# Kernel optimization log

Hardware: AMD Instinct MI355X
Metric: run time of the kernel (lower is better)

## Reference

```python
import jax, jax.numpy as jnp
import numpy as np

B, T, N, F_OUT, K, HID = 8, 12, 4096, 12, 3, 64
HALF = T // 2


def setup_inputs() -> dict:
    key = jax.random.key(0)
    ks = jax.random.split(key, 7)
    return {
        "x": jax.random.normal(ks[0], (B, T, N, 1), jnp.float32),
        "adj": jax.random.normal(ks[1], (K, N, N), jnp.float32) / np.float32(np.sqrt(N)),
        "cheb_w": jax.random.normal(ks[2], (HID, K), jnp.float32) / np.float32(np.sqrt(K)),
        "gcn_w": jax.random.normal(ks[3], (F_OUT, T, 1, HID), jnp.float32) / np.float32(np.sqrt(T * HID)),
        "gcn_b": jnp.zeros((F_OUT,), jnp.float32),
        "glu1_w": jax.random.normal(ks[4], (F_OUT, HALF, 3, 3), jnp.float32) / np.float32(np.sqrt(HALF * 9)),
        "glu1_b": jnp.zeros((F_OUT,), jnp.float32),
        "glu2_w": jax.random.normal(ks[5], (F_OUT, HALF, 3, 3), jnp.float32) / np.float32(np.sqrt(HALF * 9)),
        "glu2_b": jnp.zeros((F_OUT,), jnp.float32),
    }


def _dilated_conv(x, w, b):
    # Conv2d(kernel=3, dilation=2, padding=2) on (B, C, N, 1)
    y = jax.lax.conv_general_dilated(
        x, w, window_strides=(1, 1), padding=((2, 2), (2, 2)),
        rhs_dilation=(2, 2), dimension_numbers=("NCHW", "OIHW", "NCHW"))
    return y + b[None, :, None, None]


def reference(x, adj, cheb_w, gcn_w, gcn_b, glu1_w, glu1_b, glu2_w, glu2_b):
    # --- ChebConv (vectorized over the per-channel Python loop) ---
    # x: (B, T, N, 1), adj: (K, N, N) -> y: (B, T, N, K)
    y = jnp.einsum("knm,btm->btnk", adj, x[..., 0])
    # Linear(K -> HID, no bias) + ReLU -> cheb: (B, T, N, HID)
    cheb = jax.nn.relu(jnp.einsum("btnk,ok->btno", y, cheb_w))
    # --- gcn_conv: Conv2d(T -> F_OUT, kernel (1, HID)) -> (B, F_OUT, N, 1) ---
    sgc = jnp.einsum("btnj,otj->bon", cheb, gcn_w[:, :, 0, :]) + gcn_b[None, :, None]
    sgc = sgc[..., None]
    # --- GLU path: split history in half, dilated convs, a * sigmoid(g) ---
    x_u, x_v = x[:, :HALF], x[:, HALF:]
    a = _dilated_conv(x_u, glu1_w, glu1_b)
    g = _dilated_conv(x_v, glu2_w, glu2_b)
    x_glu = a * jax.nn.sigmoid(g)
    return x_glu + sgc
```

## Files before the change

### kernel.cpp

```cpp
#include <hip/hip_runtime.h>
#include <hip/hip_bf16.h>
#include <math.h>

#define NNODES 4096
#define NCOLS  96
#define NROWS  12288

typedef __attribute__((ext_vector_type(8))) short short8;
typedef __attribute__((ext_vector_type(4))) float float4v;

__global__ void probe_dtype(const unsigned int* __restrict__ aw, int* __restrict__ flag) {
    int tid = threadIdx.x;
    unsigned w = aw[tid];
    unsigned e = (w >> 7) & 0xffu;
    bool insane = (e >= 0xC0u) || (e <= 0x30u);
    unsigned long long m = __ballot(insane);
    if (tid == 0) flag[0] = (__popcll(m) >= 16) ? 1 : 0;
}

__device__ __forceinline__ float ldf(const void* p, size_t i, int isf32) {
    return isf32 ? ((const float*)p)[i]
                 : __bfloat162float(((const __hip_bfloat16*)p)[i]);
}

__device__ __forceinline__ void ld8(float* d, const void* p, size_t e, int isf32) {
    if (isf32) {
        const float4* s = (const float4*)((const float*)p + e);
        float4 f0 = s[0], f1 = s[1];
        d[0] = f0.x; d[1] = f0.y; d[2] = f0.z; d[3] = f0.w;
        d[4] = f1.x; d[5] = f1.y; d[6] = f1.z; d[7] = f1.w;
    } else {
        const __hip_bfloat16* s = (const __hip_bfloat16*)p + e;
#pragma unroll
        for (int j = 0; j < 8; j++) d[j] = __bfloat162float(s[j]);
    }
}

__device__ __forceinline__ void st4bf(__hip_bfloat16* d, float4 f) {
    __align__(8) __hip_bfloat16 t[4];
    t[0] = __float2bfloat16(f.x); t[1] = __float2bfloat16(f.y);
    t[2] = __float2bfloat16(f.z); t[3] = __float2bfloat16(f.w);
    *(uint2*)d = *(const uint2*)t;
}

__global__ __launch_bounds__(256) void gemm_y(
    const void* __restrict__ adjv, const void* __restrict__ xv,
    float* __restrict__ yws, const int* __restrict__ flag)
{
    __shared__ __align__(16) __hip_bfloat16 As[64][72];
    __shared__ __align__(16) __hip_bfloat16 Xs[96][72];

    const int tid = threadIdx.x;
    const int isf32 = flag[0];
    const size_t row0 = (size_t)blockIdx.x * 64;

    const int wv = tid >> 6;
    const int ln = tid & 63;
    const int fr = ln & 15;
    const int fq = ln >> 4;

    float4v acc[6];
#pragma unroll
    for (int i = 0; i < 6; i++) acc[i] = (float4v){0.f, 0.f, 0.f, 0.f};

    if (isf32) {
        const float* adjf = (const float*)adjv;
        const float* xf   = (const float*)xv;
        const int ar = tid >> 2;
        const int ac = (tid & 3) * 16;

        float4 ra[4], rx[6];
#pragma unroll
        for (int i = 0; i < 4; i++)
            ra[i] = *(const float4*)(adjf + (row0 + ar) * NNODES + ac + i * 4);
#pragma unroll
        for (int s = 0; s < 6; s++) {
            int idx = tid + s * 256;
            int r = idx >> 4, c = (idx & 15) * 4;
            rx[s] = *(const float4*)(xf + (size_t)r * NNODES + c);
        }

        for (int kk = 0; kk < NNODES; kk += 64) {
            __syncthreads();
#pragma unroll
            for (int i = 0; i < 4; i++) st4bf(&As[ar][ac + i * 4], ra[i]);
#pragma unroll
            for (int s = 0; s < 6; s++) {
                int idx = tid + s * 256;
                int r = idx >> 4, c = (idx & 15) * 4;
                st4bf(&Xs[r][c], rx[s]);
            }
            if (kk + 64 < NNODES) {
                int kn = kk + 64;
#pragma unroll
                for (int i = 0; i < 4; i++)
                    ra[i] = *(const float4*)(adjf + (row0 + ar) * NNODES + kn + ac + i * 4);
#pragma unroll
                for (int s = 0; s < 6; s++) {
                    int idx = tid + s * 256;
                    int r = idx >> 4, c = (idx & 15) * 4;
                    rx[s] = *(const float4*)(xf + (size_t)r * NNODES + kn + c);
                }
            }
            __syncthreads();
#pragma unroll
            for (int kq = 0; kq < 2; kq++) {
                short8 a = *(const short8*)(&As[wv * 16 + fr][kq * 32 + fq * 8]);
#pragma unroll
                for (int ct = 0; ct < 6; ct++) {
                    short8 b = *(const short8*)(&Xs[ct * 16 + fr][kq * 32 + fq * 8]);
                    acc[ct] = __builtin_amdgcn_mfma_f32_16x16x32_bf16(a, b, acc[ct], 0, 0, 0);
                }
            }
        }
    } else {
        const __hip_bfloat16* adjb = (const __hip_bfloat16*)adjv;
        const __hip_bfloat16* xb   = (const __hip_bfloat16*)xv;
        const int ar = tid >> 2;
        const int ac = (tid & 3) * 16;
        for (int kk = 0; kk < NNODES; kk += 64) {
            __syncthreads();
            *(uint4*)(&As[ar][ac]) =
                *(const uint4*)(adjb + (row0 + ar) * NNODES + kk + ac);
            *(uint4*)(&As[ar][ac + 8]) =
                *(const uint4*)(adjb + (row0 + ar) * NNODES + kk + ac + 8);
#pragma unroll
            for (int s = 0; s < 3; s++) {
                int idx = tid + s * 256;
                int r = idx >> 3, c = (idx & 7) * 8;
                *(uint4*)(&Xs[r][c]) =
                    *(const uint4*)(xb + (size_t)r * NNODES + kk + c);
            }
            __syncthreads();
#pragma unroll
            for (int kq = 0; kq < 2; kq++) {
                short8 a = *(const short8*)(&As[wv * 16 + fr][kq * 32 + fq * 8]);
#pragma unroll
                for (int ct = 0; ct < 6; ct++) {
                    short8 b = *(const short8*)(&Xs[ct * 16 + fr][kq * 32 + fq * 8]);
                    acc[ct] = __builtin_amdgcn_mfma_f32_16x16x32_bf16(a, b, acc[ct], 0, 0, 0);
                }
            }
        }
    }

#pragma unroll
    for (int ct = 0; ct < 6; ct++)
#pragma unroll
        for (int rg = 0; rg < 4; rg++) {
            size_t r = row0 + wv * 16 + fq * 4 + rg;
            yws[r * NCOLS + ct * 16 + fr] = acc[ct][rg];
        }
}

__global__ __launch_bounds__(64) void epilogue_kernel(
    const void* __restrict__ xv, const float* __restrict__ yws,
    const void* __restrict__ chebv, const void* __restrict__ gcnwv,
    const void* __restrict__ gcnbv, const void* __restrict__ g1wv,
    const void* __restrict__ g1bv, const void* __restrict__ g2wv,
    const void* __restrict__ g2bv,
    float* __restrict__ out, const int* __restrict__ flag)
{
    __shared__ float gwL[9216];
    __shared__ float cwL[192];
    __shared__ float w1L[216];
    __shared__ float w2L[216];
    __shared__ float wbL[36];

    const int tid = threadIdx.x;
    const int isf32 = flag[0];

    for (int i = tid; i < 9216; i += 64) {
        int o = i / 768, t = (i / 64) % 12, j = i % 64;
        gwL[t * 768 + j * 12 + o] = ldf(gcnwv, i, isf32);
    }
    for (int i = tid; i < 192; i += 64) cwL[i] = ldf(chebv, i, isf32);
    for (int i = tid; i < 216; i += 64) {
        w1L[i] = ldf(g1wv, (size_t)i * 3 + 1, isf32);
        w2L[i] = ldf(g2wv, (size_t)i * 3 + 1, isf32);
    }
    if (tid < 12) {
        wbL[tid]      = ldf(gcnbv, tid, isf32);
        wbL[12 + tid] = ldf(g1bv, tid, isf32);
        wbL[24 + tid] = ldf(g2bv, tid, isf32);
    }
    __syncthreads();

    const int g = blockIdx.x * 64 + tid;
    const int b = g >> 12;
    const int n = g & (NNODES - 1);

    float y[36];
#pragma unroll
    for (int k = 0; k < 3; k++) {
        const float* yp = yws + ((size_t)(k * NNODES + n)) * NCOLS + b * 12;
        float4 q0 = *(const float4*)(yp);
        float4 q1 = *(const float4*)(yp + 4);
        float4 q2 = *(const float4*)(yp + 8);
        y[k*12+0]=q0.x; y[k*12+1]=q0.y; y[k*12+2] =q0.z; y[k*12+3] =q0.w;
        y[k*12+4]=q1.x; y[k*12+5]=q1.y; y[k*12+6] =q1.z; y[k*12+7] =q1.w;
        y[k*12+8]=q2.x; y[k*12+9]=q2.y; y[k*12+10]=q2.z; y[k*12+11]=q2.w;
    }

    float sg[12];
#pragma unroll
    for (int o = 0; o < 12; o++) sg[o] = wbL[o];
    for (int t = 0; t < 12; t++) {
        const float y0 = y[t], y1 = y[12 + t], y2 = y[24 + t];
        const float* gwt = gwL + t * 768;
#pragma unroll 4
        for (int j = 0; j < 64; j++) {
            float h = y0 * cwL[j * 3] + y1 * cwL[j * 3 + 1] + y2 * cwL[j * 3 + 2];
            h = fmaxf(h, 0.f);
#pragma unroll
            for (int o = 0; o < 12; o++) sg[o] += h * gwt[j * 12 + o];
        }
    }

    float xa[18], xg[18];
#pragma unroll
    for (int c = 0; c < 6; c++)
#pragma unroll
        for (int kh = 0; kh < 3; kh++) {
            int m = n + 2 * kh - 2;
            bool ok = ((unsigned)m < (unsigned)NNODES);
            xa[c * 3 + kh] = ok ? ldf(xv, ((size_t)(b * 12 + c)) * NNODES + m, isf32) : 0.f;
            xg[c * 3 + kh] = ok ? ldf(xv, ((size_t)(b * 12 + c + 6)) * NNODES + m, isf32) : 0.f;
        }

#pragma unroll
    for (int o = 0; o < 12; o++) {
        float av = wbL[12 + o], gv = wbL[24 + o];
#pragma unroll
        for (int i = 0; i < 18; i++) {
            av += xa[i] * w1L[o * 18 + i];
            gv += xg[i] * w2L[o * 18 + i];
        }
        float s = 1.f / (1.f + expf(-gv));
        out[((size_t)(b * 12 + o)) * NNODES + n] = av * s + sg[o];
    }
}

__global__ __launch_bounds__(64) void fused_simple(
    const void* __restrict__ xv, const void* __restrict__ adjv,
    const void* __restrict__ chebv, const void* __restrict__ gcnwv,
    const void* __restrict__ gcnbv, const void* __restrict__ g1wv,
    const void* __restrict__ g1bv, const void* __restrict__ g2wv,
    const void* __restrict__ g2bv,
    float* __restrict__ out, const int* __restrict__ flag)
{
    __shared__ float gwL[9216];
    __shared__ float cwL[192];
    __shared__ float w1L[216];
    __shared__ float w2L[216];
    __shared__ float wbL[36];

    const int tid = threadIdx.x;
    const int isf32 = flag[0];

    for (int i = tid; i < 9216; i += 64) {
        int o = i / 768, t = (i / 64) % 12, j = i % 64;
        gwL[t * 768 + j * 12 + o] = ldf(gcnwv, i, isf32);
    }
    for (int i = tid; i < 192; i += 64) cwL[i] = ldf(chebv, i, isf32);
    for (int i = tid; i < 216; i += 64) {
        w1L[i] = ldf(g1wv, (size_t)i * 3 + 1, isf32);
        w2L[i] = ldf(g2wv, (size_t)i * 3 + 1, isf32);
    }
    if (tid < 12) {
        wbL[tid]      = ldf(gcnbv, tid, isf32);
        wbL[12 + tid] = ldf(g1bv, tid, isf32);
        wbL[24 + tid] = ldf(g2bv, tid, isf32);
    }
    __syncthreads();

    const int g = blockIdx.x * 64 + tid;
    const int b = g >> 12;
    const int n = g & (NNODES - 1);

    float y[3][12];
#pragma unroll
    for (int k = 0; k < 3; k++)
#pragma unroll
        for (int t = 0; t < 12; t++) y[k][t] = 0.f;

    for (int m0 = 0; m0 < NNODES; m0 += 8) {
        float a0[8], a1[8], a2[8];
        ld8(a0, adjv, ((size_t)(0 * NNODES + n)) * NNODES + m0, isf32);
        ld8(a1, adjv, ((size_t)(1 * NNODES + n)) * NNODES + m0, isf32);
        ld8(a2, adjv, ((size_t)(2 * NNODES + n)) * NNODES + m0, isf32);
#pragma unroll
        for (int t = 0; t < 12; t++) {
            float x8[8];
            ld8(x8, xv, ((size_t)(b * 12 + t)) * NNODES + m0, isf32);
#pragma unroll
            for (int j = 0; j < 8; j++) {
                y[0][t] += a0[j] * x8[j];
                y[1][t] += a1[j] * x8[j];
                y[2][t] += a2[j] * x8[j];
            }
        }
    }

    float sg[12];
#pragma unroll
    for (int o = 0; o < 12; o++) sg[o] = wbL[o];
    for (int t = 0; t < 12; t++) {
        const float y0 = y[0][t], y1 = y[1][t], y2 = y[2][t];
        const float* gwt = gwL + t * 768;
#pragma unroll 4
        for (int j = 0; j < 64; j++) {
            float h = y0 * cwL[j * 3] + y1 * cwL[j * 3 + 1] + y2 * cwL[j * 3 + 2];
            h = fmaxf(h, 0.f);
#pragma unroll
            for (int o = 0; o < 12; o++) sg[o] += h * gwt[j * 12 + o];
        }
    }

    float xa[18], xg[18];
#pragma unroll
    for (int c = 0; c < 6; c++)
#pragma unroll
        for (int kh = 0; kh < 3; kh++) {
            int m = n + 2 * kh - 2;
            bool ok = ((unsigned)m < (unsigned)NNODES);
            xa[c * 3 + kh] = ok ? ldf(xv, ((size_t)(b * 12 + c)) * NNODES + m, isf32) : 0.f;
            xg[c * 3 + kh] = ok ? ldf(xv, ((size_t)(b * 12 + c + 6)) * NNODES + m, isf32) : 0.f;
        }

#pragma unroll
    for (int o = 0; o < 12; o++) {
        float av = wbL[12 + o], gv = wbL[24 + o];
#pragma unroll
        for (int i = 0; i < 18; i++) {
            av += xa[i] * w1L[o * 18 + i];
            gv += xg[i] * w2L[o * 18 + i];
        }
        float s = 1.f / (1.f + expf(-gv));
        out[((size_t)(b * 12 + o)) * NNODES + n] = av * s + sg[o];
    }
}

extern "C" void kernel_launch(void* const* d_in, const int* in_sizes, int n_in,
                              void* d_out, int out_size, void* d_ws, size_t ws_size,
                              hipStream_t stream)
{
    int* flag = (int*)d_ws;
    float* yws = (float*)((char*)d_ws + 64);
    const size_t need = 64 + (size_t)NROWS * NCOLS * 4;

    hipLaunchKernelGGL(probe_dtype, dim3(1), dim3(64), 0, stream,
                       (const unsigned int*)d_in[1], flag);

    if (ws_size >= need) {
        hipLaunchKernelGGL(gemm_y, dim3(192), dim3(256), 0, stream,
                           d_in[1], d_in[0], yws, flag);
        hipLaunchKernelGGL(epilogue_kernel, dim3(512), dim3(64), 0, stream,
                           d_in[0], yws, d_in[2], d_in[3], d_in[4],
                           d_in[5], d_in[6], d_in[7], d_in[8],
                           (float*)d_out, flag);
    } else {
        hipLaunchKernelGGL(fused_simple, dim3(512), dim3(64), 0, stream,
                           d_in[0], d_in[1], d_in[2], d_in[3], d_in[4],
                           d_in[5], d_in[6], d_in[7], d_in[8],
                           (float*)d_out, flag);
    }
}
```

Baseline: 413.8 us.

## Retile adjacency GEMM with swizzled double-buffered LDS and split epilogue timesteps across lanes

The GEMM block height drops from 64 to 48 rows, giving 256 blocks of 3 waves instead of 192 blocks of 4. The LDS tiles become double-buffered with an XOR swizzle, which removes one barrier per K step and avoids bank conflicts. The epilogue now gives each output pixel four lanes, each handling three timesteps of the Chebyshev/GCN reduction, combined with xor shuffles. Each lane also computes three of the GLU outputs, so there is four times more parallelism in the previously under-occupied epilogue. The cost is cross-lane shuffles, redundant loads of the GLU inputs across the four lanes, and a narrower GEMM tile that reuses the X tile less.

```diff
diff --git a/kernel.cpp b/kernel.cpp
--- a/kernel.cpp
+++ b/kernel.cpp
@@ -5,6 +5,8 @@
 #define NNODES 4096
 #define NCOLS  96
 #define NROWS  12288
+#define BM     48
+#define BK     64
 
 typedef __attribute__((ext_vector_type(8))) short short8;
 typedef __attribute__((ext_vector_type(4))) float float4v;
@@ -36,23 +38,25 @@
     }
 }
 
-__device__ __forceinline__ void st4bf(__hip_bfloat16* d, float4 f) {
-    __align__(8) __hip_bfloat16 t[4];
-    t[0] = __float2bfloat16(f.x); t[1] = __float2bfloat16(f.y);
-    t[2] = __float2bfloat16(f.z); t[3] = __float2bfloat16(f.w);
-    *(uint2*)d = *(const uint2*)t;
-}
-
-__global__ __launch_bounds__(256) void gemm_y(
+__device__ __forceinline__ short8 cvt8(float4 a, float4 b) {
+    union { short8 v; __hip_bfloat16 h[8]; } u;
+    u.h[0] = __float2bfloat16(a.x); u.h[1] = __float2bfloat16(a.y);
+    u.h[2] = __float2bfloat16(a.z); u.h[3] = __float2bfloat16(a.w);
+    u.h[4] = __float2bfloat16(b.x); u.h[5] = __float2bfloat16(b.y);
+    u.h[6] = __float2bfloat16(b.z); u.h[7] = __float2bfloat16(b.w);
+    return u.v;
+}
+
+__global__ __launch_bounds__(192) void gemm_y(
     const void* __restrict__ adjv, const void* __restrict__ xv,
     float* __restrict__ yws, const int* __restrict__ flag)
 {
-    __shared__ __align__(16) __hip_bfloat16 As[64][72];
-    __shared__ __align__(16) __hip_bfloat16 Xs[96][72];
+    __shared__ __align__(16) short8 As[2][BM * 8];
+    __shared__ __align__(16) short8 Xs[2][96 * 8];
 
     const int tid = threadIdx.x;
     const int isf32 = flag[0];
-    const size_t row0 = (size_t)blockIdx.x * 64;
+    const size_t row0 = (size_t)blockIdx.x * BM;
 
     const int wv = tid >> 6;
     const int ln = tid & 63;
@@ -63,84 +67,106 @@
 #pragma unroll
     for (int i = 0; i < 6; i++) acc[i] = (float4v){0.f, 0.f, 0.f, 0.f};
 
+    int arow[2], acol[2], aslot[2];
+#pragma unroll
+    for (int s = 0; s < 2; s++) {
+        int g = tid + s * 192;
+        arow[s] = g >> 3; acol[s] = (g & 7) * 8;
+        aslot[s] = (g >> 3) * 8 + ((g & 7) ^ ((g >> 3) & 7));
+    }
+    int xrow[4], xcol[4], xslot[4];
+#pragma unroll
+    for (int s = 0; s < 4; s++) {
+        int g = tid + s * 192;
+        xrow[s] = g >> 3; xcol[s] = (g & 7) * 8;
+        xslot[s] = (g >> 3) * 8 + ((g & 7) ^ ((g >> 3) & 7));
+    }
+
     if (isf32) {
         const float* adjf = (const float*)adjv;
         const float* xf   = (const float*)xv;
-        const int ar = tid >> 2;
-        const int ac = (tid & 3) * 16;
-
-        float4 ra[4], rx[6];
-#pragma unroll
-        for (int i = 0; i < 4; i++)
-            ra[i] = *(const float4*)(adjf + (row0 + ar) * NNODES + ac + i * 4);
-#pragma unroll
-        for (int s = 0; s < 6; s++) {
-            int idx = tid + s * 256;
-            int r = idx >> 4, c = (idx & 15) * 4;
-            rx[s] = *(const float4*)(xf + (size_t)r * NNODES + c);
-        }
-
-        for (int kk = 0; kk < NNODES; kk += 64) {
+
+        float4 pa[2][2], px[4][2];
+#pragma unroll
+        for (int s = 0; s < 2; s++) {
+            const float* p = adjf + (row0 + arow[s]) * NNODES + acol[s];
+            pa[s][0] = *(const float4*)p; pa[s][1] = *(const float4*)(p + 4);
+        }
+#pragma unroll
+        for (int s = 0; s < 4; s++) {
+            const float* p = xf + (size_t)xrow[s] * NNODES + xcol[s];
+            px[s][0] = *(const float4*)p; px[s][1] = *(const float4*)(p + 4);
+        }
+
+        int buf = 0;
+        for (int kk = 0; kk < NNODES; kk += BK) {
+#pragma unroll
+            for (int s = 0; s < 2; s++) As[buf][aslot[s]] = cvt8(pa[s][0], pa[s][1]);
+#pragma unroll
+            for (int s = 0; s < 4; s++) Xs[buf][xslot[s]] = cvt8(px[s][0], px[s][1]);
+            if (kk + BK < NNODES) {
+                const int kn = kk + BK;
+#pragma unroll
+                for (int s = 0; s < 2; s++) {
+                    const float* p = adjf + (row0 + arow[s]) * NNODES + kn + acol[s];
+                    pa[s][0] = *(const float4*)p; pa[s][1] = *(const float4*)(p + 4);
+                }
+#pragma unroll
+                for (int s = 0; s < 4; s++) {
+                    const float* p = xf + (size_t)xrow[s] * NNODES + kn + xcol[s];
+                    px[s][0] = *(const float4*)p; px[s][1] = *(const float4*)(p + 4);
+                }
+            }
             __syncthreads();
 #pragma unroll
-            for (int i = 0; i < 4; i++) st4bf(&As[ar][ac + i * 4], ra[i]);
-#pragma unroll
-            for (int s = 0; s < 6; s++) {
-                int idx = tid + s * 256;
-                int r = idx >> 4, c = (idx & 15) * 4;
-                st4bf(&Xs[r][c], rx[s]);
-            }
-            if (kk + 64 < NNODES) {
-                int kn = kk + 64;
-#pragma unroll
-                for (int i = 0; i < 4; i++)
-                    ra[i] = *(const float4*)(adjf + (row0 + ar) * NNODES + kn + ac + i * 4);
-#pragma unroll
-                for (int s = 0; s < 6; s++) {
-                    int idx = tid + s * 256;
-                    int r = idx >> 4, c = (idx & 15) * 4;
-                    rx[s] = *(const float4*)(xf + (size_t)r * NNODES + kn + c);
+            for (int kq = 0; kq < 2; kq++) {
+                short8 a = As[buf][(wv * 16 + fr) * 8 + ((kq * 4 + fq) ^ (fr & 7))];
+#pragma unroll
+                for (int ct = 0; ct < 6; ct++) {
+                    short8 bfr = Xs[buf][(ct * 16 + fr) * 8 + ((kq * 4 + fq) ^ (fr & 7))];
+                    acc[ct] = __builtin_amdgcn_mfma_f32_16x16x32_bf16(a, bfr, acc[ct], 0, 0, 0);
                 }
             }
-            __syncthreads();
-#pragma unroll
-            for (int kq = 0; kq < 2; kq++) {
-                short8 a = *(const short8*)(&As[wv * 16 + fr][kq * 32 + fq * 8]);
-#pragma unroll
-                for (int ct = 0; ct < 6; ct++) {
-                    short8 b = *(const short8*)(&Xs[ct * 16 + fr][kq * 32 + fq * 8]);
-                    acc[ct] = __builtin_amdgcn_mfma_f32_16x16x32_bf16(a, b, acc[ct], 0, 0, 0);
-                }
-            }
+            buf ^= 1;
         }
     } else {
         const __hip_bfloat16* adjb = (const __hip_bfloat16*)adjv;
         const __hip_bfloat16* xb   = (const __hip_bfloat16*)xv;
-        const int ar = tid >> 2;
-        const int ac = (tid & 3) * 16;
-        for (int kk = 0; kk < NNODES; kk += 64) {
+
+        uint4 pa[2], px[4];
+#pragma unroll
+        for (int s = 0; s < 2; s++)
+            pa[s] = *(const uint4*)(adjb + (row0 + arow[s]) * NNODES + acol[s]);
+#pragma unroll
+        for (int s = 0; s < 4; s++)
+            px[s] = *(const uint4*)(xb + (size_t)xrow[s] * NNODES + xcol[s]);
+
+        int buf = 0;
+        for (int kk = 0; kk < NNODES; kk += BK) {
+#pragma unroll
+            for (int s = 0; s < 2; s++) *(uint4*)&As[buf][aslot[s]] = pa[s];
+#pragma unroll
+            for (int s = 0; s < 4; s++) *(uint4*)&Xs[buf][xslot[s]] = px[s];
+            if (kk + BK < NNODES) {
+                const int kn = kk + BK;
+#pragma unroll
+                for (int s = 0; s < 2; s++)
+                    pa[s] = *(const uint4*)(adjb + (row0 + arow[s]) * NNODES + kn + acol[s]);
+#pragma unroll
+                for (int s = 0; s < 4; s++)
+                    px[s] = *(const uint4*)(xb + (size_t)xrow[s] * NNODES + kn + xcol[s]);
+            }
             __syncthreads();
-            *(uint4*)(&As[ar][ac]) =
-                *(const uint4*)(adjb + (row0 + ar) * NNODES + kk + ac);
-            *(uint4*)(&As[ar][ac + 8]) =
-                *(const uint4*)(adjb + (row0 + ar) * NNODES + kk + ac + 8);
-#pragma unroll
-            for (int s = 0; s < 3; s++) {
-                int idx = tid + s * 256;
-                int r = idx >> 3, c = (idx & 7) * 8;
-                *(uint4*)(&Xs[r][c]) =
-                    *(const uint4*)(xb + (size_t)r * NNODES + kk + c);
-            }
-            __syncthreads();
 #pragma unroll
             for (int kq = 0; kq < 2; kq++) {
-                short8 a = *(const short8*)(&As[wv * 16 + fr][kq * 32 + fq * 8]);
+                short8 a = As[buf][(wv * 16 + fr) * 8 + ((kq * 4 + fq) ^ (fr & 7))];
 #pragma unroll
                 for (int ct = 0; ct < 6; ct++) {
-                    short8 b = *(const short8*)(&Xs[ct * 16 + fr][kq * 32 + fq * 8]);
-                    acc[ct] = __builtin_amdgcn_mfma_f32_16x16x32_bf16(a, b, acc[ct], 0, 0, 0);
+                    short8 bfr = Xs[buf][(ct * 16 + fr) * 8 + ((kq * 4 + fq) ^ (fr & 7))];
+                    acc[ct] = __builtin_amdgcn_mfma_f32_16x16x32_bf16(a, bfr, acc[ct], 0, 0, 0);
                 }
             }
+            buf ^= 1;
         }
     }
 
@@ -153,7 +179,7 @@
         }
 }
 
-__global__ __launch_bounds__(64) void epilogue_kernel(
+__global__ __launch_bounds__(256) void epilogue_kernel(
     const void* __restrict__ xv, const float* __restrict__ yws,
     const void* __restrict__ chebv, const void* __restrict__ gcnwv,
     const void* __restrict__ gcnbv, const void* __restrict__ g1wv,
@@ -170,14 +196,14 @@
     const int tid = threadIdx.x;
     const int isf32 = flag[0];
 
-    for (int i = tid; i < 9216; i += 64) {
+    for (int i = tid; i < 9216; i += 256) {
         int o = i / 768, t = (i / 64) % 12, j = i % 64;
         gwL[t * 768 + j * 12 + o] = ldf(gcnwv, i, isf32);
     }
-    for (int i = tid; i < 192; i += 64) cwL[i] = ldf(chebv, i, isf32);
-    for (int i = tid; i < 216; i += 64) {
-        w1L[i] = ldf(g1wv, (size_t)i * 3 + 1, isf32);
-        w2L[i] = ldf(g2wv, (size_t)i * 3 + 1, isf32);
+    if (tid < 192) cwL[tid] = ldf(chebv, tid, isf32);
+    if (tid < 216) {
+        w1L[tid] = ldf(g1wv, (size_t)tid * 3 + 1, isf32);
+        w2L[tid] = ldf(g2wv, (size_t)tid * 3 + 1, isf32);
     }
     if (tid < 12) {
         wbL[tid]      = ldf(gcnbv, tid, isf32);
@@ -186,28 +212,26 @@
     }
     __syncthreads();
 
-    const int g = blockIdx.x * 64 + tid;
-    const int b = g >> 12;
-    const int n = g & (NNODES - 1);
-
-    float y[36];
+    const int gid = blockIdx.x * 256 + tid;
+    const int pr  = gid >> 2;
+    const int tq  = gid & 3;
+    const int b = pr >> 12;
+    const int n = pr & (NNODES - 1);
+
+    float yk[3][3];
 #pragma unroll
     for (int k = 0; k < 3; k++) {
-        const float* yp = yws + ((size_t)(k * NNODES + n)) * NCOLS + b * 12;
-        float4 q0 = *(const float4*)(yp);
-        float4 q1 = *(const float4*)(yp + 4);
-        float4 q2 = *(const float4*)(yp + 8);
-        y[k*12+0]=q0.x; y[k*12+1]=q0.y; y[k*12+2] =q0.z; y[k*12+3] =q0.w;
-        y[k*12+4]=q1.x; y[k*12+5]=q1.y; y[k*12+6] =q1.z; y[k*12+7] =q1.w;
-        y[k*12+8]=q2.x; y[k*12+9]=q2.y; y[k*12+10]=q2.z; y[k*12+11]=q2.w;
+        const float* yp = yws + ((size_t)(k * NNODES + n)) * NCOLS + b * 12 + tq * 3;
+        yk[k][0] = yp[0]; yk[k][1] = yp[1]; yk[k][2] = yp[2];
     }
 
     float sg[12];
 #pragma unroll
-    for (int o = 0; o < 12; o++) sg[o] = wbL[o];
-    for (int t = 0; t < 12; t++) {
-        const float y0 = y[t], y1 = y[12 + t], y2 = y[24 + t];
-        const float* gwt = gwL + t * 768;
+    for (int o = 0; o < 12; o++) sg[o] = 0.f;
+#pragma unroll
+    for (int i = 0; i < 3; i++) {
+        const float y0 = yk[0][i], y1 = yk[1][i], y2 = yk[2][i];
+        const float* gwt = gwL + (tq * 3 + i) * 768;
 #pragma unroll 4
         for (int j = 0; j < 64; j++) {
             float h = y0 * cwL[j * 3] + y1 * cwL[j * 3 + 1] + y2 * cwL[j * 3 + 2];
@@ -215,6 +239,11 @@
 #pragma unroll
             for (int o = 0; o < 12; o++) sg[o] += h * gwt[j * 12 + o];
         }
+    }
+#pragma unroll
+    for (int o = 0; o < 12; o++) {
+        sg[o] += __shfl_xor(sg[o], 1);
+        sg[o] += __shfl_xor(sg[o], 2);
     }
 
     float xa[18], xg[18];
@@ -229,15 +258,16 @@
         }
 
 #pragma unroll
-    for (int o = 0; o < 12; o++) {
+    for (int i = 0; i < 3; i++) {
+        const int o = tq * 3 + i;
         float av = wbL[12 + o], gv = wbL[24 + o];
 #pragma unroll
-        for (int i = 0; i < 18; i++) {
-            av += xa[i] * w1L[o * 18 + i];
-            gv += xg[i] * w2L[o * 18 + i];
+        for (int q = 0; q < 18; q++) {
+            av += xa[q] * w1L[o * 18 + q];
+            gv += xg[q] * w2L[o * 18 + q];
         }
         float s = 1.f / (1.f + expf(-gv));
-        out[((size_t)(b * 12 + o)) * NNODES + n] = av * s + sg[o];
+        out[((size_t)(b * 12 + o)) * NNODES + n] = av * s + sg[o] + wbL[o];
     }
 }
 
@@ -353,9 +383,9 @@
                        (const unsigned int*)d_in[1], flag);
 
     if (ws_size >= need) {
-        hipLaunchKernelGGL(gemm_y, dim3(192), dim3(256), 0, stream,
+        hipLaunchKernelGGL(gemm_y, dim3(256), dim3(192), 0, stream,
                            d_in[1], d_in[0], yws, flag);
-        hipLaunchKernelGGL(epilogue_kernel, dim3(512), dim3(64), 0, stream,
+        hipLaunchKernelGGL(epilogue_kernel, dim3(512), dim3(256), 0, stream,
                            d_in[0], yws, d_in[2], d_in[3], d_in[4],
                            d_in[5], d_in[6], d_in[7], d_in[8],
                            (float*)d_out, flag);
```

New measurement: 367.6 us. -11.2%, faster.
